# Kernel optimization log

Hardware: AMD Instinct MI355X
Metric: run time of the kernel (lower is better)

Reference implementation:

```python
import jax, jax.numpy as jnp
import numpy as np

N_NODES = 100000
N_EDGES = 3200000
HID = 16
MP_ROUNDS = 3


def _mlp(w1, b1, w2, b2, x):
    # channels-first MLP applied per edge/node: x is [C_in, E]
    h = jax.nn.relu(w1 @ x + b1[:, None])
    return w2 @ h + b2[:, None]


def setup_inputs() -> dict:
    key = jax.random.key(0)
    ks = jax.random.split(key, 20)
    s = lambda k, shp: jax.random.normal(k, shp, dtype=jnp.float32) * 0.1
    inp = {
        "nodes": jax.random.normal(ks[0], (N_NODES,), dtype=jnp.float32),
        "edges_init": jax.random.normal(ks[1], (N_EDGES,), dtype=jnp.float32),
        "senders": jax.random.randint(ks[2], (N_EDGES,), 0, N_NODES, dtype=jnp.int32),
        "receivers": jax.random.randint(ks[3], (N_EDGES,), 0, N_NODES, dtype=jnp.int32),
        # EdgeEncoder: 1 -> HID -> HID
        "enc_w1": s(ks[4], (HID, 1)), "enc_b1": jnp.zeros((HID,), jnp.float32),
        "enc_w2": s(ks[5], (HID, HID)), "enc_b2": jnp.zeros((HID,), jnp.float32),
        # Node update MLP: (1 + 2*HID) -> HID -> 1  (shared across rounds)
        "node_w1": s(ks[6], (HID, 1 + 2 * HID)), "node_b1": jnp.zeros((HID,), jnp.float32),
        "node_w2": s(ks[7], (1, HID)), "node_b2": jnp.zeros((1,), jnp.float32),
        # Edge update MLP: (HID + 2) -> HID -> HID  (shared across rounds)
        "edge_w1": s(ks[8], (HID, HID + 2)), "edge_b1": jnp.zeros((HID,), jnp.float32),
        "edge_w2": s(ks[9], (HID, HID)), "edge_b2": jnp.zeros((HID,), jnp.float32),
        # EdgeDecoder: HID -> HID -> 1
        "dec_w1": s(ks[10], (HID, HID)), "dec_b1": jnp.zeros((HID,), jnp.float32),
        "dec_w2": s(ks[11], (1, HID)), "dec_b2": jnp.zeros((1,), jnp.float32),
        "alpha": jnp.float32(0.1),
    }
    return inp


def reference(nodes, edges_init, senders, receivers,
              enc_w1, enc_b1, enc_w2, enc_b2,
              node_w1, node_b1, node_w2, node_b2,
              edge_w1, edge_b1, edge_w2, edge_b2,
              dec_w1, dec_b1, dec_w2, dec_b2, alpha):
    n_nodes = nodes.shape[0]
    norm = jnp.abs(edges_init).max()
    e = edges_init / norm                      # [E]
    e = _mlp(enc_w1, enc_b1, enc_w2, enc_b2, e[None, :])   # [HID, E]
    for _ in range(MP_ROUNDS):                 # shared-weight MP blocks
        # gather/scatter: aggregate edge features to nodes
        agg_s = jax.ops.segment_sum(e.T, senders, num_segments=n_nodes).T     # [HID, N]
        agg_r = jax.ops.segment_sum(e.T, receivers, num_segments=n_nodes).T   # [HID, N]
        node_in = jnp.concatenate([nodes[None, :], agg_s, agg_r], axis=0)     # [1+2H, N]
        nodes = _mlp(node_w1, node_b1, node_w2, node_b2, node_in)[0]          # [N]
        edge_in = jnp.concatenate([e, nodes[senders][None, :], nodes[receivers][None, :]], axis=0)  # [H+2, E]
        e = _mlp(edge_w1, edge_b1, edge_w2, edge_b2, edge_in)                 # [HID, E]
    e = _mlp(dec_w1, dec_b1, dec_w2, dec_b2, e)[0]          # [E]
    low_tri_data = edges_init + alpha * (e * norm)          # L = L + alpha*GNN(L)
    return low_tri_data
```

## Files before the change

kernel.cpp:

```cpp
#include <hip/hip_runtime.h>
#include <hip/hip_bf16.h>

#define N_NODES 100000
#define N_EDGES 3200000
#define HID 16
#define MAXDEG 128
#define NPART 8
#define PART_NODES (N_NODES / NPART)

static constexpr int BLK = 256;

__device__ __forceinline__ float frelu(float x) { return fmaxf(x, 0.f); }
__device__ __forceinline__ float bf2f(unsigned short u) {
  return __uint_as_float(((unsigned int)u) << 16);
}

union E16 {
  float4 f4[2];
  __hip_bfloat16 h[16];
};

__global__ __launch_bounds__(256) void k_norm(const float* __restrict__ edges,
                                              unsigned int* __restrict__ normbits) {
  float m = 0.f;
  for (int i = blockIdx.x * blockDim.x + threadIdx.x; i < N_EDGES;
       i += gridDim.x * blockDim.x)
    m = fmaxf(m, fabsf(edges[i]));
#pragma unroll
  for (int off = 32; off > 0; off >>= 1)
    m = fmaxf(m, __shfl_down(m, off, 64));
  __shared__ float smax[BLK / 64];
  if ((threadIdx.x & 63) == 0) smax[threadIdx.x >> 6] = m;
  __syncthreads();
  if (threadIdx.x == 0) {
    float b = smax[0];
#pragma unroll
    for (int w = 1; w < BLK / 64; ++w) b = fmaxf(b, smax[w]);
    atomicMax(normbits, __float_as_uint(b));
  }
}

__global__ __launch_bounds__(256) void k_build(const int* __restrict__ senders,
                                               const int* __restrict__ receivers,
                                               int* __restrict__ count,
                                               int* __restrict__ ell) {
  int p = blockIdx.x & (NPART - 1);
  int q = blockIdx.x >> 3;
  int nblk = gridDim.x >> 3;
  int lo = p * PART_NODES, hi = lo + PART_NODES;
  for (int i = q * blockDim.x + threadIdx.x; i < N_EDGES;
       i += nblk * blockDim.x) {
    int s = __builtin_nontemporal_load(&senders[i]);
    if (s >= lo && s < hi) {
      int slot = atomicAdd(&count[s], 1);
      if (slot < MAXDEG) ell[(size_t)s * MAXDEG + slot] = (i << 1);
    }
    int r = __builtin_nontemporal_load(&receivers[i]);
    if (r >= lo && r < hi) {
      int slot = atomicAdd(&count[r], 1);
      if (slot < MAXDEG) ell[(size_t)r * MAXDEG + slot] = (i << 1) | 1;
    }
  }
}

__global__ __launch_bounds__(256) void k_encode(
    const float* __restrict__ edges, const float* __restrict__ w1,
    const float* __restrict__ b1, const float* __restrict__ w2,
    const float* __restrict__ b2, const unsigned int* __restrict__ normbits,
    __hip_bfloat16* __restrict__ e) {
  int i = blockIdx.x * blockDim.x + threadIdx.x;
  if (i >= N_EDGES) return;
  float norm = __uint_as_float(*normbits);
  float x = edges[i] / norm;
  float h[HID];
#pragma unroll
  for (int j = 0; j < HID; ++j) h[j] = frelu(fmaf(w1[j], x, b1[j]));
  E16 o;
#pragma unroll
  for (int j = 0; j < HID; ++j) {
    float acc = b2[j];
#pragma unroll
    for (int k = 0; k < HID; ++k) acc = fmaf(w2[j * HID + k], h[k], acc);
    o.h[j] = __float2bfloat16(acc);
  }
  float4* ep = (float4*)(e + (size_t)i * HID);
  ep[0] = o.f4[0];
  ep[1] = o.f4[1];
}

__global__ __launch_bounds__(256) void k_gather(
    const unsigned short* __restrict__ e, const int* __restrict__ count,
    const int* __restrict__ ell, float* __restrict__ agg) {
  int wave = (blockIdx.x * blockDim.x + threadIdx.x) >> 6;
  int lane = threadIdx.x & 63;
  if (wave >= N_NODES) return;
  int n = wave;
  int deg = count[n];
  if (deg > MAXDEG) deg = MAXDEG;
  const int* lst = ell + (size_t)n * MAXDEG;
  int sub = lane & 3;
  float as0 = 0.f, as1 = 0.f, as2 = 0.f, as3 = 0.f;
  float ar0 = 0.f, ar1 = 0.f, ar2 = 0.f, ar3 = 0.f;
  for (int k0 = 0; k0 < deg; k0 += 64) {
    int ent = lst[k0 + lane];
#pragma unroll
    for (int t = 0; t < 4; ++t) {
      int slot = k0 + t * 16 + (lane >> 2);
      int entry = __shfl(ent, t * 16 + (lane >> 2), 64);
      bool ok = slot < deg;
      int edge = ok ? (entry >> 1) : 0;
      ushort4 raw = *(const ushort4*)(e + (size_t)edge * HID + sub * 4);
      float v0 = bf2f(raw.x), v1 = bf2f(raw.y), v2 = bf2f(raw.z),
            v3 = bf2f(raw.w);
      bool recv = ok && (entry & 1);
      bool send = ok && !(entry & 1);
      as0 += send ? v0 : 0.f;  as1 += send ? v1 : 0.f;
      as2 += send ? v2 : 0.f;  as3 += send ? v3 : 0.f;
      ar0 += recv ? v0 : 0.f;  ar1 += recv ? v1 : 0.f;
      ar2 += recv ? v2 : 0.f;  ar3 += recv ? v3 : 0.f;
    }
  }
#pragma unroll
  for (int off = 32; off >= 4; off >>= 1) {
    as0 += __shfl_down(as0, off, 64);  as1 += __shfl_down(as1, off, 64);
    as2 += __shfl_down(as2, off, 64);  as3 += __shfl_down(as3, off, 64);
    ar0 += __shfl_down(ar0, off, 64);  ar1 += __shfl_down(ar1, off, 64);
    ar2 += __shfl_down(ar2, off, 64);  ar3 += __shfl_down(ar3, off, 64);
  }
  if (lane < 4) {
    *(float4*)(agg + (size_t)n * 32 + lane * 4) = make_float4(as0, as1, as2, as3);
    *(float4*)(agg + (size_t)n * 32 + 16 + lane * 4) = make_float4(ar0, ar1, ar2, ar3);
  }
}

__global__ __launch_bounds__(256) void k_node(
    const float* __restrict__ nodes_in, const float* __restrict__ agg,
    const float* __restrict__ w1, const float* __restrict__ b1,
    const float* __restrict__ w2, const float* __restrict__ b2,
    float* __restrict__ nodes_out) {
  int n = blockIdx.x * blockDim.x + threadIdx.x;
  if (n >= N_NODES) return;
  float x0 = nodes_in[n];
  const float4* ap = (const float4*)(agg + (size_t)n * 32);
  float av[32];
#pragma unroll
  for (int q = 0; q < 8; ++q) {
    float4 v = ap[q];
    av[q * 4 + 0] = v.x;
    av[q * 4 + 1] = v.y;
    av[q * 4 + 2] = v.z;
    av[q * 4 + 3] = v.w;
  }
  float out = b2[0];
#pragma unroll
  for (int j = 0; j < HID; ++j) {
    float acc = fmaf(w1[j * 33], x0, b1[j]);
#pragma unroll
    for (int k = 0; k < 32; ++k) acc = fmaf(w1[j * 33 + 1 + k], av[k], acc);
    out = fmaf(w2[j], frelu(acc), out);
  }
  nodes_out[n] = out;
}

__global__ __launch_bounds__(256) void k_edge(
    __hip_bfloat16* __restrict__ e, const int* __restrict__ senders,
    const int* __restrict__ receivers, const float* __restrict__ nodes,
    const float* __restrict__ w1, const float* __restrict__ b1,
    const float* __restrict__ w2, const float* __restrict__ b2) {
  int i = blockIdx.x * blockDim.x + threadIdx.x;
  if (i >= N_EDGES) return;
  int s = senders[i], r = receivers[i];
  float ns = nodes[s], nr = nodes[r];
  float4* ep = (float4*)(e + (size_t)i * HID);
  E16 in;
  in.f4[0] = ep[0];
  in.f4[1] = ep[1];
  float x[HID];
#pragma unroll
  for (int k = 0; k < HID; ++k) x[k] = __bfloat162float(in.h[k]);
  float h[HID];
#pragma unroll
  for (int j = 0; j < HID; ++j) {
    float acc = b1[j];
#pragma unroll
    for (int k = 0; k < HID; ++k) acc = fmaf(w1[j * 18 + k], x[k], acc);
    acc = fmaf(w1[j * 18 + 16], ns, acc);
    acc = fmaf(w1[j * 18 + 17], nr, acc);
    h[j] = frelu(acc);
  }
  E16 o;
#pragma unroll
  for (int j = 0; j < HID; ++j) {
    float acc = b2[j];
#pragma unroll
    for (int k = 0; k < HID; ++k) acc = fmaf(w2[j * HID + k], h[k], acc);
    o.h[j] = __float2bfloat16(acc);
  }
  ep[0] = o.f4[0];
  ep[1] = o.f4[1];
}

__global__ __launch_bounds__(256) void k_final(
    const __hip_bfloat16* __restrict__ e, const int* __restrict__ senders,
    const int* __restrict__ receivers, const float* __restrict__ nodes,
    const float* __restrict__ w1, const float* __restrict__ b1,
    const float* __restrict__ w2, const float* __restrict__ b2,
    const float* __restrict__ dw1, const float* __restrict__ db1,
    const float* __restrict__ dw2, const float* __restrict__ db2,
    const float* __restrict__ edges_init,
    const unsigned int* __restrict__ normbits, const float* __restrict__ alpha,
    float* __restrict__ out) {
  int i = blockIdx.x * blockDim.x + threadIdx.x;
  if (i >= N_EDGES) return;
  int s = senders[i], r = receivers[i];
  float ns = nodes[s], nr = nodes[r];
  const float4* ep = (const float4*)(e + (size_t)i * HID);
  E16 in;
  in.f4[0] = ep[0];
  in.f4[1] = ep[1];
  float x[HID];
#pragma unroll
  for (int k = 0; k < HID; ++k) x[k] = __bfloat162float(in.h[k]);
  float h[HID];
#pragma unroll
  for (int j = 0; j < HID; ++j) {
    float acc = b1[j];
#pragma unroll
    for (int k = 0; k < HID; ++k) acc = fmaf(w1[j * 18 + k], x[k], acc);
    acc = fmaf(w1[j * 18 + 16], ns, acc);
    acc = fmaf(w1[j * 18 + 17], nr, acc);
    h[j] = frelu(acc);
  }
  float e3[HID];
#pragma unroll
  for (int j = 0; j < HID; ++j) {
    float acc = b2[j];
#pragma unroll
    for (int k = 0; k < HID; ++k) acc = fmaf(w2[j * HID + k], h[k], acc);
    e3[j] = acc;
  }
  float d = db2[0];
#pragma unroll
  for (int j = 0; j < HID; ++j) {
    float acc = db1[j];
#pragma unroll
    for (int k = 0; k < HID; ++k) acc = fmaf(dw1[j * HID + k], e3[k], acc);
    d = fmaf(dw2[j], frelu(acc), d);
  }
  float norm = __uint_as_float(*normbits);
  out[i] = fmaf(alpha[0], d * norm, edges_init[i]);
}

extern "C" void kernel_launch(void* const* d_in, const int* in_sizes, int n_in,
                              void* d_out, int out_size, void* d_ws,
                              size_t ws_size, hipStream_t stream) {
  const float* nodes0 = (const float*)d_in[0];
  const float* edges0 = (const float*)d_in[1];
  const int* senders = (const int*)d_in[2];
  const int* receivers = (const int*)d_in[3];
  const float* enc_w1 = (const float*)d_in[4];
  const float* enc_b1 = (const float*)d_in[5];
  const float* enc_w2 = (const float*)d_in[6];
  const float* enc_b2 = (const float*)d_in[7];
  const float* node_w1 = (const float*)d_in[8];
  const float* node_b1 = (const float*)d_in[9];
  const float* node_w2 = (const float*)d_in[10];
  const float* node_b2 = (const float*)d_in[11];
  const float* edge_w1 = (const float*)d_in[12];
  const float* edge_b1 = (const float*)d_in[13];
  const float* edge_w2 = (const float*)d_in[14];
  const float* edge_b2 = (const float*)d_in[15];
  const float* dec_w1 = (const float*)d_in[16];
  const float* dec_b1 = (const float*)d_in[17];
  const float* dec_w2 = (const float*)d_in[18];
  const float* dec_b2 = (const float*)d_in[19];
  const float* alpha = (const float*)d_in[20];

  char* ws = (char*)d_ws;
  __hip_bfloat16* e = (__hip_bfloat16*)ws;
  float* agg = (float*)(ws + (size_t)N_EDGES * HID * 2);
  float* nb1 = agg + (size_t)N_NODES * 32;
  float* nb2 = nb1 + N_NODES;
  unsigned int* normbits = (unsigned int*)(nb2 + N_NODES);
  int* count = (int*)(normbits + 16);
  int* ell = count + N_NODES;

  const int egrid = N_EDGES / BLK;
  const int ngrid = (N_NODES + BLK - 1) / BLK;
  const int ggrid = (N_NODES * 64) / BLK;
  const int bgrid = 3520;

  hipMemsetAsync(normbits, 0, sizeof(unsigned int), stream);
  hipMemsetAsync(count, 0, (size_t)N_NODES * sizeof(int), stream);
  k_norm<<<512, BLK, 0, stream>>>(edges0, normbits);
  k_build<<<bgrid, BLK, 0, stream>>>(senders, receivers, count, ell);
  k_encode<<<egrid, BLK, 0, stream>>>(edges0, enc_w1, enc_b1, enc_w2, enc_b2,
                                      normbits, e);
  k_gather<<<ggrid, BLK, 0, stream>>>((const unsigned short*)e, count, ell, agg);
  k_node<<<ngrid, BLK, 0, stream>>>(nodes0, agg, node_w1, node_b1, node_w2,
                                    node_b2, nb1);
  k_edge<<<egrid, BLK, 0, stream>>>(e, senders, receivers, nb1, edge_w1,
                                    edge_b1, edge_w2, edge_b2);
  k_gather<<<ggrid, BLK, 0, stream>>>((const unsigned short*)e, count, ell, agg);
  k_node<<<ngrid, BLK, 0, stream>>>(nb1, agg, node_w1, node_b1, node_w2,
                                    node_b2, nb2);
  k_edge<<<egrid, BLK, 0, stream>>>(e, senders, receivers, nb2, edge_w1,
                                    edge_b1, edge_w2, edge_b2);
  k_gather<<<ggrid, BLK, 0, stream>>>((const unsigned short*)e, count, ell, agg);
  k_node<<<ngrid, BLK, 0, stream>>>(nb2, agg, node_w1, node_b1, node_w2,
                                    node_b2, nb1);
  k_final<<<egrid, BLK, 0, stream>>>(e, senders, receivers, nb1, edge_w1,
                                     edge_b1, edge_w2, edge_b2, dec_w1, dec_b1,
                                     dec_w2, dec_b2, edges0, normbits, alpha,
                                     (float*)d_out);
}
```

Before: 1.051 ms.

## Split ELL build into per-XCD sub-partitions with vectorized index loads

The adjacency build kernel now has each XCD group process four node sub-partitions in sequence instead of one partition. Each pass keeps the set of count and ell rows it touches small enough to stay cache-resident. Sender and receiver indices are now read as int4 vectors. The trade-off is that the edge index arrays are streamed four times per block instead of once.

```diff
diff --git a/kernel.cpp b/kernel.cpp
--- a/kernel.cpp
+++ b/kernel.cpp
@@ -5,10 +5,14 @@
 #define N_EDGES 3200000
 #define HID 16
 #define MAXDEG 128
-#define NPART 8
-#define PART_NODES (N_NODES / NPART)
+#define NXCD 8
+#define SUBP 4
+#define NPARTS (NXCD * SUBP)
+#define PART_NODES (N_NODES / NPARTS)
 
 static constexpr int BLK = 256;
+
+typedef int v4i __attribute__((ext_vector_type(4)));
 
 __device__ __forceinline__ float frelu(float x) { return fmaxf(x, 0.f); }
 __device__ __forceinline__ float bf2f(unsigned short u) {
@@ -44,21 +48,32 @@
                                                const int* __restrict__ receivers,
                                                int* __restrict__ count,
                                                int* __restrict__ ell) {
-  int p = blockIdx.x & (NPART - 1);
+  int xcd = blockIdx.x & (NXCD - 1);
   int q = blockIdx.x >> 3;
   int nblk = gridDim.x >> 3;
-  int lo = p * PART_NODES, hi = lo + PART_NODES;
-  for (int i = q * blockDim.x + threadIdx.x; i < N_EDGES;
-       i += nblk * blockDim.x) {
-    int s = __builtin_nontemporal_load(&senders[i]);
-    if (s >= lo && s < hi) {
-      int slot = atomicAdd(&count[s], 1);
-      if (slot < MAXDEG) ell[(size_t)s * MAXDEG + slot] = (i << 1);
-    }
-    int r = __builtin_nontemporal_load(&receivers[i]);
-    if (r >= lo && r < hi) {
-      int slot = atomicAdd(&count[r], 1);
-      if (slot < MAXDEG) ell[(size_t)r * MAXDEG + slot] = (i << 1) | 1;
+  const v4i* s4p = (const v4i*)senders;
+  const v4i* r4p = (const v4i*)receivers;
+  const int nvec = N_EDGES / 4;
+  for (int sub = 0; sub < SUBP; ++sub) {
+    int part = xcd * SUBP + sub;
+    int lo = part * PART_NODES, hi = lo + PART_NODES;
+    for (int v = q * blockDim.x + threadIdx.x; v < nvec; v += nblk * blockDim.x) {
+      v4i s4 = __builtin_nontemporal_load(s4p + v);
+      v4i r4 = __builtin_nontemporal_load(r4p + v);
+      int base = v * 4;
+#pragma unroll
+      for (int t = 0; t < 4; ++t) {
+        int s = s4[t];
+        if (s >= lo && s < hi) {
+          int slot = atomicAdd(&count[s], 1);
+          if (slot < MAXDEG) ell[(size_t)s * MAXDEG + slot] = ((base + t) << 1);
+        }
+        int r = r4[t];
+        if (r >= lo && r < hi) {
+          int slot = atomicAdd(&count[r], 1);
+          if (slot < MAXDEG) ell[(size_t)r * MAXDEG + slot] = ((base + t) << 1) | 1;
+        }
+      }
     }
   }
 }
```

After: 1.166 ms. 1.11x slower.

## Replace partitioned atomic ELL build with two-pass shared-memory bucketing

Applied to the files above, without the earlier changes.

The adjacency (ELL) build changes. The old version scanned all edges once per node partition and did global atomics per edge. The new version bins the packed (local node, edge id) records into 391 buckets of 256 nodes, staging them in shared memory and flushing them in chunks. A second kernel then builds each bucket's per-node lists in LDS and writes them out coalesced. This cuts global atomic traffic and repeated input reads, at the cost of an extra records buffer. It also relies on fixed capacities (32-entry staging, 18432 per bucket, 126 per node) that hold only for well-spread indices.

```diff
diff --git a/kernel.cpp b/kernel.cpp
--- a/kernel.cpp
+++ b/kernel.cpp
@@ -5,8 +5,10 @@
 #define N_EDGES 3200000
 #define HID 16
 #define MAXDEG 128
-#define NPART 8
-#define PART_NODES (N_NODES / NPART)
+#define NBUCK 391
+#define SCAP 32
+#define FLUSH_T 12
+#define BCAP 18432
 
 static constexpr int BLK = 256;
 
@@ -40,26 +42,95 @@
   }
 }
 
-__global__ __launch_bounds__(256) void k_build(const int* __restrict__ senders,
-                                               const int* __restrict__ receivers,
-                                               int* __restrict__ count,
-                                               int* __restrict__ ell) {
-  int p = blockIdx.x & (NPART - 1);
-  int q = blockIdx.x >> 3;
-  int nblk = gridDim.x >> 3;
-  int lo = p * PART_NODES, hi = lo + PART_NODES;
-  for (int i = q * blockDim.x + threadIdx.x; i < N_EDGES;
-       i += nblk * blockDim.x) {
-    int s = __builtin_nontemporal_load(&senders[i]);
-    if (s >= lo && s < hi) {
-      int slot = atomicAdd(&count[s], 1);
-      if (slot < MAXDEG) ell[(size_t)s * MAXDEG + slot] = (i << 1);
-    }
-    int r = __builtin_nontemporal_load(&receivers[i]);
-    if (r >= lo && r < hi) {
-      int slot = atomicAdd(&count[r], 1);
-      if (slot < MAXDEG) ell[(size_t)r * MAXDEG + slot] = (i << 1) | 1;
-    }
+__global__ __launch_bounds__(256) void k_bucket(
+    const int* __restrict__ senders, const int* __restrict__ receivers,
+    int* __restrict__ cursor, unsigned int* __restrict__ records) {
+  __shared__ int cnt[NBUCK];
+  __shared__ unsigned int stag[NBUCK * SCAP];
+  for (int j = threadIdx.x; j < NBUCK; j += BLK) cnt[j] = 0;
+  __syncthreads();
+  const int nbatch = N_EDGES / BLK;
+  int lane = threadIdx.x & 63;
+  int wave = threadIdx.x >> 6;
+  for (int batch = blockIdx.x; batch < nbatch; batch += gridDim.x) {
+    int i = batch * BLK + threadIdx.x;
+    int s = senders[i], r = receivers[i];
+    {
+      int b = s >> 8;
+      unsigned rec = ((unsigned)(s & 255) << 23) | (unsigned)(i << 1);
+      int slot = atomicAdd(&cnt[b], 1);
+      if (slot < SCAP) stag[b * SCAP + slot] = rec;
+    }
+    {
+      int b = r >> 8;
+      unsigned rec = ((unsigned)(r & 255) << 23) | (unsigned)((i << 1) | 1);
+      int slot = atomicAdd(&cnt[b], 1);
+      if (slot < SCAP) stag[b * SCAP + slot] = rec;
+    }
+    __syncthreads();
+    for (int b = wave; b < NBUCK; b += BLK / 64) {
+      int c = cnt[b];
+      if (c >= FLUSH_T) {
+        c = c > SCAP ? SCAP : c;
+        int base = 0;
+        if (lane == 0) base = atomicAdd(&cursor[b], c);
+        base = __shfl(base, 0, 64);
+        if (lane < c) {
+          unsigned idx = (unsigned)(base + lane);
+          if (idx < BCAP) records[(size_t)b * BCAP + idx] = stag[b * SCAP + lane];
+        }
+        if (lane == 0) cnt[b] = 0;
+      }
+    }
+    __syncthreads();
+  }
+  for (int b = wave; b < NBUCK; b += BLK / 64) {
+    int c = cnt[b];
+    if (c > 0) {
+      c = c > SCAP ? SCAP : c;
+      int base = 0;
+      if (lane == 0) base = atomicAdd(&cursor[b], c);
+      base = __shfl(base, 0, 64);
+      if (lane < c) {
+        unsigned idx = (unsigned)(base + lane);
+        if (idx < BCAP) records[(size_t)b * BCAP + idx] = stag[b * SCAP + lane];
+      }
+    }
+  }
+}
+
+__global__ __launch_bounds__(256) void k_csr(
+    const unsigned int* __restrict__ records, const int* __restrict__ cursor,
+    int* __restrict__ count, int* __restrict__ ell) {
+  __shared__ int cnt[128];
+  __shared__ int el[128 * 126];
+  int b = blockIdx.x;
+  int T = cursor[b];
+  if (T > BCAP) T = BCAP;
+  const unsigned int* rp = records + (size_t)b * BCAP;
+  for (int half = 0; half < 2; ++half) {
+    if (threadIdx.x < 128) cnt[threadIdx.x] = 0;
+    __syncthreads();
+    for (int t = threadIdx.x; t < T; t += BLK) {
+      unsigned rec = rp[t];
+      int local = (int)(rec >> 23);
+      if ((local >> 7) == half) {
+        int l7 = local & 127;
+        int slot = atomicAdd(&cnt[l7], 1);
+        if (slot < 126) el[l7 * 126 + slot] = (int)(rec & 0x7FFFFFu);
+      }
+    }
+    __syncthreads();
+    size_t gbase = ((size_t)b * 256 + half * 128) * MAXDEG;
+    for (int t = threadIdx.x; t < 128 * 126; t += BLK) {
+      int node = t / 126, slot = t - node * 126;
+      ell[gbase + (size_t)node * MAXDEG + slot] = el[t];
+    }
+    if (threadIdx.x < 128) {
+      int c = cnt[threadIdx.x];
+      count[b * 256 + half * 128 + threadIdx.x] = c > 126 ? 126 : c;
+    }
+    __syncthreads();
   }
 }
 
@@ -282,18 +353,20 @@
   float* nb1 = agg + (size_t)N_NODES * 32;
   float* nb2 = nb1 + N_NODES;
   unsigned int* normbits = (unsigned int*)(nb2 + N_NODES);
-  int* count = (int*)(normbits + 16);
-  int* ell = count + N_NODES;
+  int* cursor = (int*)(normbits + 16);
+  int* count = cursor + 512;
+  int* ell = count + (NBUCK * 256);
+  unsigned int* records = (unsigned int*)(ell + (size_t)NBUCK * 256 * MAXDEG);
 
   const int egrid = N_EDGES / BLK;
   const int ngrid = (N_NODES + BLK - 1) / BLK;
   const int ggrid = (N_NODES * 64) / BLK;
-  const int bgrid = 3520;
 
   hipMemsetAsync(normbits, 0, sizeof(unsigned int), stream);
-  hipMemsetAsync(count, 0, (size_t)N_NODES * sizeof(int), stream);
+  hipMemsetAsync(cursor, 0, NBUCK * sizeof(int), stream);
   k_norm<<<512, BLK, 0, stream>>>(edges0, normbits);
-  k_build<<<bgrid, BLK, 0, stream>>>(senders, receivers, count, ell);
+  k_bucket<<<768, BLK, 0, stream>>>(senders, receivers, cursor, records);
+  k_csr<<<NBUCK, BLK, 0, stream>>>(records, cursor, count, ell);
   k_encode<<<egrid, BLK, 0, stream>>>(edges0, enc_w1, enc_b1, enc_w2, enc_b2,
                                       normbits, e);
   k_gather<<<ggrid, BLK, 0, stream>>>((const unsigned short*)e, count, ell, agg);
```

New measurement: 1.562 ms. +48.5%, slower.

## Process two nodes per wave in gather with unrolled 64-slot ELL fast path

Applied to the files above, without the earlier changes.

The gather kernel now assigns each half-wave (32 lanes) to one node, so a wave handles two nodes and the grid shrinks by half. The first 64 ELL slots are processed in a fully unrolled loop, and a second block runs only if either node has degree above 64. ELL index loads become nontemporal, and the edge-list build loads become ordinary cached loads. The aim is to cut wasted lanes and loop overhead for typical degrees of about 64 while raising memory-level parallelism. The cost is more divergence when the two nodes' degrees differ.

```diff
diff --git a/kernel.cpp b/kernel.cpp
--- a/kernel.cpp
+++ b/kernel.cpp
@@ -50,12 +50,12 @@
   int lo = p * PART_NODES, hi = lo + PART_NODES;
   for (int i = q * blockDim.x + threadIdx.x; i < N_EDGES;
        i += nblk * blockDim.x) {
-    int s = __builtin_nontemporal_load(&senders[i]);
+    int s = senders[i];
     if (s >= lo && s < hi) {
       int slot = atomicAdd(&count[s], 1);
       if (slot < MAXDEG) ell[(size_t)s * MAXDEG + slot] = (i << 1);
     }
-    int r = __builtin_nontemporal_load(&receivers[i]);
+    int r = receivers[i];
     if (r >= lo && r < hi) {
       int slot = atomicAdd(&count[r], 1);
       if (slot < MAXDEG) ell[(size_t)r * MAXDEG + slot] = (i << 1) | 1;
@@ -93,43 +93,68 @@
     const int* __restrict__ ell, float* __restrict__ agg) {
   int wave = (blockIdx.x * blockDim.x + threadIdx.x) >> 6;
   int lane = threadIdx.x & 63;
-  if (wave >= N_NODES) return;
-  int n = wave;
+  int half = lane >> 5;
+  int l32 = lane & 31;
+  int sub = l32 & 3;
+  int j8 = l32 >> 2;
+  int n = wave * 2 + half;
+  if (n >= N_NODES) return;
   int deg = count[n];
   if (deg > MAXDEG) deg = MAXDEG;
   const int* lst = ell + (size_t)n * MAXDEG;
-  int sub = lane & 3;
-  float as0 = 0.f, as1 = 0.f, as2 = 0.f, as3 = 0.f;
-  float ar0 = 0.f, ar1 = 0.f, ar2 = 0.f, ar3 = 0.f;
-  for (int k0 = 0; k0 < deg; k0 += 64) {
-    int ent = lst[k0 + lane];
-#pragma unroll
-    for (int t = 0; t < 4; ++t) {
-      int slot = k0 + t * 16 + (lane >> 2);
-      int entry = __shfl(ent, t * 16 + (lane >> 2), 64);
+  int ent0 = __builtin_nontemporal_load(lst + l32);
+  int ent1 = __builtin_nontemporal_load(lst + 32 + l32);
+  float as[4] = {0.f, 0.f, 0.f, 0.f};
+  float ar[4] = {0.f, 0.f, 0.f, 0.f};
+#pragma unroll
+  for (int t = 0; t < 8; ++t) {
+    int slot = t * 8 + j8;
+    int entry = __shfl(t < 4 ? ent0 : ent1, half * 32 + (t & 3) * 8 + j8, 64);
+    bool ok = slot < deg;
+    int edge = ok ? (entry >> 1) : 0;
+    ushort4 raw = *(const ushort4*)(e + (size_t)edge * HID + sub * 4);
+    float v[4] = {bf2f(raw.x), bf2f(raw.y), bf2f(raw.z), bf2f(raw.w)};
+    bool recv = ok && (entry & 1);
+    bool send = ok && !(entry & 1);
+#pragma unroll
+    for (int c = 0; c < 4; ++c) {
+      as[c] += send ? v[c] : 0.f;
+      ar[c] += recv ? v[c] : 0.f;
+    }
+  }
+  if (__any(deg > 64)) {
+    int ent2 = __builtin_nontemporal_load(lst + 64 + l32);
+    int ent3 = __builtin_nontemporal_load(lst + 96 + l32);
+#pragma unroll
+    for (int t = 0; t < 8; ++t) {
+      int slot = 64 + t * 8 + j8;
+      int entry = __shfl(t < 4 ? ent2 : ent3, half * 32 + (t & 3) * 8 + j8, 64);
       bool ok = slot < deg;
       int edge = ok ? (entry >> 1) : 0;
       ushort4 raw = *(const ushort4*)(e + (size_t)edge * HID + sub * 4);
-      float v0 = bf2f(raw.x), v1 = bf2f(raw.y), v2 = bf2f(raw.z),
-            v3 = bf2f(raw.w);
+      float v[4] = {bf2f(raw.x), bf2f(raw.y), bf2f(raw.z), bf2f(raw.w)};
       bool recv = ok && (entry & 1);
       bool send = ok && !(entry & 1);
-      as0 += send ? v0 : 0.f;  as1 += send ? v1 : 0.f;
-      as2 += send ? v2 : 0.f;  as3 += send ? v3 : 0.f;
-      ar0 += recv ? v0 : 0.f;  ar1 += recv ? v1 : 0.f;
-      ar2 += recv ? v2 : 0.f;  ar3 += recv ? v3 : 0.f;
-    }
-  }
-#pragma unroll
-  for (int off = 32; off >= 4; off >>= 1) {
-    as0 += __shfl_down(as0, off, 64);  as1 += __shfl_down(as1, off, 64);
-    as2 += __shfl_down(as2, off, 64);  as3 += __shfl_down(as3, off, 64);
-    ar0 += __shfl_down(ar0, off, 64);  ar1 += __shfl_down(ar1, off, 64);
-    ar2 += __shfl_down(ar2, off, 64);  ar3 += __shfl_down(ar3, off, 64);
-  }
-  if (lane < 4) {
-    *(float4*)(agg + (size_t)n * 32 + lane * 4) = make_float4(as0, as1, as2, as3);
-    *(float4*)(agg + (size_t)n * 32 + 16 + lane * 4) = make_float4(ar0, ar1, ar2, ar3);
+#pragma unroll
+      for (int c = 0; c < 4; ++c) {
+        as[c] += send ? v[c] : 0.f;
+        ar[c] += recv ? v[c] : 0.f;
+      }
+    }
+  }
+#pragma unroll
+  for (int off = 16; off >= 4; off >>= 1) {
+#pragma unroll
+    for (int c = 0; c < 4; ++c) {
+      as[c] += __shfl_down(as[c], off, 64);
+      ar[c] += __shfl_down(ar[c], off, 64);
+    }
+  }
+  if (l32 < 4) {
+    *(float4*)(agg + (size_t)n * 32 + l32 * 4) =
+        make_float4(as[0], as[1], as[2], as[3]);
+    *(float4*)(agg + (size_t)n * 32 + 16 + l32 * 4) =
+        make_float4(ar[0], ar[1], ar[2], ar[3]);
   }
 }
 
@@ -287,7 +312,7 @@
 
   const int egrid = N_EDGES / BLK;
   const int ngrid = (N_NODES + BLK - 1) / BLK;
-  const int ggrid = (N_NODES * 64) / BLK;
+  const int ggrid = N_NODES / 8;
   const int bgrid = 3520;
 
   hipMemsetAsync(normbits, 0, sizeof(unsigned int), stream);
```

Measured after the change: 1.030 ms. -2.1%, faster.
